# Kernel optimization log

Hardware: AMD Instinct MI355X
Metric: run time of the kernel (lower is better)

Reference implementation:

```python
import jax, jax.numpy as jnp
import numpy as np

C_RGB, C_EV, K = 64, 32, 3
PAD = K // 2
MID = 32


def setup_inputs() -> dict:
    key = jax.random.key(0)
    ks = jax.random.split(key, 6)
    B, H, W = 4, 256, 256
    rgb_feature = jax.random.normal(ks[0], (B, C_RGB, H, W), dtype=jnp.float32)
    event_feature = jax.random.normal(ks[1], (B, C_EV, H, W), dtype=jnp.float32)
    cin = C_RGB + C_EV
    # 1x1 conv weights stored as [out, in] (kaiming-ish scale)
    W1 = jax.random.normal(ks[2], (MID, cin), dtype=jnp.float32) / np.sqrt(cin)
    b1 = jnp.zeros((MID,), dtype=jnp.float32)
    W2 = jax.random.normal(ks[3], (C_RGB * K * K, MID), dtype=jnp.float32) / np.sqrt(MID)
    b2 = jnp.zeros((C_RGB * K * K,), dtype=jnp.float32)
    return {"rgb_feature": rgb_feature, "event_feature": event_feature,
            "W1": W1, "b1": b1, "W2": W2, "b2": b2}


def _extract_patches(x, k):
    # x: [B, C, H+2p, W+2p] -> [B, C, k, k, H, W]
    B, C, Hp, Wp = x.shape
    H, W = Hp - 2 * PAD, Wp - 2 * PAD
    rows = [jnp.stack([x[:, :, i:i + H, j:j + W] for j in range(k)], axis=2)
            for i in range(k)]
    return jnp.stack(rows, axis=2)  # [B, C, k, k, H, W]


def reference(rgb_feature, event_feature, W1, b1, W2, b2):
    B, C, H, W = rgb_feature.shape
    fused = jnp.concatenate([rgb_feature, event_feature], axis=1)  # [B, cin, H, W]
    # 1x1 convs as channel contractions
    h = jnp.einsum('bchw,mc->bmhw', fused, W1) + b1[None, :, None, None]
    h = jax.nn.relu(h)
    dk = jnp.einsum('bmhw,om->bohw', h, W2) + b2[None, :, None, None]
    dynamic_kernels = dk.reshape(B, C, K, K, H, W)
    rgb_padded = jnp.pad(rgb_feature, ((0, 0), (0, 0), (PAD, PAD), (PAD, PAD)), mode='reflect')
    patches = _extract_patches(rgb_padded, K)  # [B, C, K, K, H, W]
    out = jnp.einsum('bcijhw,bcijhw->bchw', patches, dynamic_kernels)
    return out
```

## Files before the change

kernel.cpp:

```cpp
#include <hip/hip_runtime.h>

#define CRGB 64
#define CEV  32
#define CIN  96
#define MID  32
#define HH   256
#define WW   256
#define HW   (HH*WW)

#define TLH 16
#define TLW 32
#define SRH 18
#define SRW 34
#define SPX (SRH*SRW)

typedef _Float16 f16x8 __attribute__((ext_vector_type(8)));
typedef _Float16 f16x4 __attribute__((ext_vector_type(4)));
typedef float    f32x4 __attribute__((ext_vector_type(4)));

#define WS_W2F 0
#define WS_W1F 36864
#define WS_B2P 43008

__global__ __launch_bounds__(256) void prep_kernel(
    const float* __restrict__ W1, const float* __restrict__ W2,
    const float* __restrict__ b2, char* __restrict__ ws)
{
    _Float16* W2f = (_Float16*)(ws + WS_W2F);
    _Float16* W1f = (_Float16*)(ws + WS_W1F);
    float*    b2p = (float*)(ws + WS_B2P);
    const int idx = blockIdx.x * 256 + threadIdx.x;
    if (idx < 18432) {
        const int e   = idx & 7;
        const int ln  = (idx >> 3) & 63;
        const int t   = idx >> 9;
        const int ij  = t % 9, cg = t / 9;
        const int c   = cg * 16 + (ln & 15);
        const int kap = (ln >> 4) * 8 + e;
        const int m   = ((kap >> 2) & 1) * 16 + (kap >> 3) * 4 + (kap & 3);
        W2f[idx] = (_Float16)W2[(c * 9 + ij) * MID + m];
    }
    if (idx < 3072) {
        const int e  = idx & 7;
        const int ln = (idx >> 3) & 63;
        const int t  = idx >> 9;
        const int ks = t >> 1, mh = t & 1;
        const int m  = mh * 16 + (ln & 15);
        const int k  = ks * 32 + (ln >> 4) * 8 + e;
        W1f[idx] = (_Float16)W1[m * CIN + k];
    }
    if (idx < 576) {
        const int cc = idx & 15;
        const int t  = idx >> 4;
        const int ij = t % 9, cg = t / 9;
        b2p[idx] = b2[(cg * 16 + cc) * 9 + ij];
    }
}

__global__ __launch_bounds__(512, 4) void fusion_mfma2(
    const float* __restrict__ rgb, const float* __restrict__ ev,
    const float* __restrict__ b1, const char* __restrict__ ws,
    float* __restrict__ out)
{
    __shared__ __align__(16) _Float16 srgb[SPX * 64];

    const int tid  = threadIdx.x;
    const int wave = tid >> 6;
    const int lane = tid & 63;
    const int l15  = lane & 15;
    const int g    = lane >> 4;

    const int bx = blockIdx.x;
    const int tc = bx & 7, tr = (bx >> 3) & 15, b = bx >> 7;
    const int px0 = tc * TLW, py0 = tr * TLH;

    const float* rgbP = rgb + (size_t)b * CRGB * HW;
    const float* evP  = ev  + (size_t)b * CEV  * HW;
    float*       outP = out + (size_t)b * CRGB * HW;

    const _Float16* W2f = (const _Float16*)(ws + WS_W2F);
    const _Float16* W1f = (const _Float16*)(ws + WS_W1F);
    const float*    b2p = (const float*)(ws + WS_B2P);

    f16x8* sv = (f16x8*)srgb;
    for (int p = tid; p < SPX; p += 512) {
        const int row = p / SRW;
        const int col = p - row * SRW;
        int gy = py0 - 1 + row; gy = gy < 0 ? 1 : (gy > HH - 1 ? HH - 2 : gy);
        int gx = px0 - 1 + col; gx = gx < 0 ? 1 : (gx > WW - 1 ? WW - 2 : gx);
        const float* src = rgbP + (size_t)gy * WW + gx;
        const int pb = p * 8, ps = p & 7;
#pragma unroll
        for (int q = 0; q < 8; ++q) {
            f16x8 v;
#pragma unroll
            for (int e = 0; e < 8; ++e)
                v[e] = (_Float16)src[(size_t)(q * 8 + e) * HW];
            sv[pb + (q ^ ps)] = v;
        }
    }

    f16x8 a1[6];
#pragma unroll
    for (int t = 0; t < 6; ++t)
        a1[t] = ((const f16x8*)W1f)[t * 64 + lane];
    const f32x4 b1v0 = *(const f32x4*)(b1 + g * 4);
    const f32x4 b1v1 = *(const f32x4*)(b1 + 16 + g * 4);

    __syncthreads();

    f16x8 bfr[4];
#pragma unroll
    for (int st = 0; st < 4; ++st) {
        const int row_l = wave * 2 + (st & 1);
        const int col   = (st >> 1) * 16 + l15;
        const int pt    = (row_l + 1) * SRW + col + 1;
        const f16x8 bk0 = sv[pt * 8 + ( g      ^ (pt & 7))];
        const f16x8 bk1 = sv[pt * 8 + ((4 + g) ^ (pt & 7))];
        const float* esrc = evP + (size_t)(py0 + row_l) * WW + (px0 + col);
        f16x8 bk2;
#pragma unroll
        for (int e = 0; e < 8; ++e)
            bk2[e] = (_Float16)esrc[(size_t)(g * 8 + e) * HW];
        f32x4 d0 = {0.f, 0.f, 0.f, 0.f}, d1 = {0.f, 0.f, 0.f, 0.f};
        d0 = __builtin_amdgcn_mfma_f32_16x16x32_f16(a1[0], bk0, d0, 0, 0, 0);
        d1 = __builtin_amdgcn_mfma_f32_16x16x32_f16(a1[1], bk0, d1, 0, 0, 0);
        d0 = __builtin_amdgcn_mfma_f32_16x16x32_f16(a1[2], bk1, d0, 0, 0, 0);
        d1 = __builtin_amdgcn_mfma_f32_16x16x32_f16(a1[3], bk1, d1, 0, 0, 0);
        d0 = __builtin_amdgcn_mfma_f32_16x16x32_f16(a1[4], bk2, d0, 0, 0, 0);
        d1 = __builtin_amdgcn_mfma_f32_16x16x32_f16(a1[5], bk2, d1, 0, 0, 0);
        f16x8 bf;
#pragma unroll
        for (int r = 0; r < 4; ++r) {
            float v0 = d0[r] + b1v0[r]; v0 = v0 > 0.f ? v0 : 0.f;
            float v1 = d1[r] + b1v1[r]; v1 = v1 > 0.f ? v1 : 0.f;
            bf[r]     = (_Float16)v0;
            bf[4 + r] = (_Float16)v1;
        }
        bfr[st] = bf;
    }

    for (int cg = 0; cg < 4; ++cg) {
        f16x8 a2[9];
        f32x4 ci[9];
#pragma unroll
        for (int ij = 0; ij < 9; ++ij) {
            a2[ij] = ((const f16x8*)W2f)[(cg * 9 + ij) * 64 + lane];
            ci[ij] = *(const f32x4*)(b2p + (cg * 9 + ij) * 16 + g * 4);
        }
        const int qs  = cg * 2 + (g >> 1);
        const int sub = g & 1;
#pragma unroll
        for (int st = 0; st < 4; ++st) {
            const int row_l = wave * 2 + (st & 1);
            const int col   = (st >> 1) * 16 + l15;
            float acc0 = 0.f, acc1 = 0.f, acc2 = 0.f, acc3 = 0.f;
#pragma unroll
            for (int ij = 0; ij < 9; ++ij) {
                const f32x4 d = __builtin_amdgcn_mfma_f32_16x16x32_f16(a2[ij], bfr[st], ci[ij], 0, 0, 0);
                const int pt = (row_l + ij / 3) * SRW + col + (ij % 3);
                const f16x4 pv = ((const f16x4*)srgb)[(pt * 8 + (qs ^ (pt & 7))) * 2 + sub];
                acc0 = fmaf(d[0], (float)pv[0], acc0);
                acc1 = fmaf(d[1], (float)pv[1], acc1);
                acc2 = fmaf(d[2], (float)pv[2], acc2);
                acc3 = fmaf(d[3], (float)pv[3], acc3);
            }
            float* op = outP + (size_t)(cg * 16 + g * 4) * HW
                             + (size_t)(py0 + row_l) * WW + (px0 + col);
            op[0]      = acc0;
            op[HW]     = acc1;
            op[2 * HW] = acc2;
            op[3 * HW] = acc3;
        }
    }
}

extern "C" void kernel_launch(void* const* d_in, const int* in_sizes, int n_in,
                              void* d_out, int out_size, void* d_ws, size_t ws_size,
                              hipStream_t stream) {
    const float* rgb = (const float*)d_in[0];
    const float* ev  = (const float*)d_in[1];
    const float* W1p = (const float*)d_in[2];
    const float* b1p = (const float*)d_in[3];
    const float* W2p = (const float*)d_in[4];
    const float* b2p = (const float*)d_in[5];
    float* out = (float*)d_out;
    char* ws = (char*)d_ws;

    hipLaunchKernelGGL(prep_kernel, dim3(72), dim3(256), 0, stream, W1p, W2p, b2p, ws);

    const int B = in_sizes[0] / (CRGB * HW);
    hipLaunchKernelGGL(fusion_mfma2, dim3(B * 128), dim3(512), 0, stream,
                       rgb, ev, b1p, ws, out);
}
```

Before: 66.14 us.

## Stage rgb tile into LDS as fp32 via direct global-to-LDS loads with 1024 threads

```diff
diff --git a/kernel.cpp b/kernel.cpp
--- a/kernel.cpp
+++ b/kernel.cpp
@@ -13,10 +13,13 @@
 #define SRH 18
 #define SRW 34
 #define SPX (SRH*SRW)
+#define QSTRIDE (SPX*4)
 
 typedef _Float16 f16x8 __attribute__((ext_vector_type(8)));
-typedef _Float16 f16x4 __attribute__((ext_vector_type(4)));
 typedef float    f32x4 __attribute__((ext_vector_type(4)));
+
+typedef const __attribute__((address_space(1))) float* gas_fp;
+typedef __attribute__((address_space(3))) float*       las_fp;
 
 #define WS_W2F 0
 #define WS_W1F 36864
@@ -57,12 +60,12 @@
     }
 }
 
-__global__ __launch_bounds__(512, 4) void fusion_mfma2(
+__global__ __launch_bounds__(1024, 1) void fusion_mfma5(
     const float* __restrict__ rgb, const float* __restrict__ ev,
     const float* __restrict__ b1, const char* __restrict__ ws,
     float* __restrict__ out)
 {
-    __shared__ __align__(16) _Float16 srgb[SPX * 64];
+    __shared__ __align__(16) float srgb[16 * QSTRIDE];
 
     const int tid  = threadIdx.x;
     const int wave = tid >> 6;
@@ -82,21 +85,24 @@
     const _Float16* W1f = (const _Float16*)(ws + WS_W1F);
     const float*    b2p = (const float*)(ws + WS_B2P);
 
-    f16x8* sv = (f16x8*)srgb;
-    for (int p = tid; p < SPX; p += 512) {
-        const int row = p / SRW;
-        const int col = p - row * SRW;
-        int gy = py0 - 1 + row; gy = gy < 0 ? 1 : (gy > HH - 1 ? HH - 2 : gy);
-        int gx = px0 - 1 + col; gx = gx < 0 ? 1 : (gx > WW - 1 ? WW - 2 : gx);
-        const float* src = rgbP + (size_t)gy * WW + gx;
-        const int pb = p * 8, ps = p & 7;
-#pragma unroll
-        for (int q = 0; q < 8; ++q) {
-            f16x8 v;
-#pragma unroll
-            for (int e = 0; e < 8; ++e)
-                v[e] = (_Float16)src[(size_t)(q * 8 + e) * HW];
-            sv[pb + (q ^ ps)] = v;
+    {
+        const int q = wave;
+        const float* chbase = rgbP + (size_t)(q * 4) * HW;
+        float* ldsbase = &srgb[q * QSTRIDE];
+#pragma unroll 4
+        for (int j = 0; j < 39; ++j) {
+            if (j < 38 || lane < 16) {
+                const int li  = j * 64 + lane;
+                const int p   = li >> 2, r = li & 3;
+                const int row = p / SRW;
+                const int col = p - row * SRW;
+                int gy = py0 - 1 + row; gy = gy < 0 ? 1 : (gy > HH - 1 ? HH - 2 : gy);
+                int gx = px0 - 1 + col; gx = gx < 0 ? 1 : (gx > WW - 1 ? WW - 2 : gx);
+                const float* gsrc = chbase + (size_t)r * HW + gy * WW + gx;
+                __builtin_amdgcn_global_load_lds(
+                    (gas_fp)(const void*)gsrc,
+                    (las_fp)(void*)(ldsbase + j * 64), 4, 0, 0);
+            }
         }
     }
 
@@ -107,28 +113,43 @@
     const f32x4 b1v0 = *(const f32x4*)(b1 + g * 4);
     const f32x4 b1v1 = *(const f32x4*)(b1 + 16 + g * 4);
 
+    const int row_l = wave;
+    f16x8 bk2[2];
+#pragma unroll
+    for (int st = 0; st < 2; ++st) {
+        const int col = st * 16 + l15;
+        const float* esrc = evP + (size_t)(py0 + row_l) * WW + (px0 + col);
+#pragma unroll
+        for (int e = 0; e < 8; ++e)
+            bk2[st][e] = (_Float16)esrc[(size_t)(g * 8 + e) * HW];
+    }
+
     __syncthreads();
 
-    f16x8 bfr[4];
-#pragma unroll
-    for (int st = 0; st < 4; ++st) {
-        const int row_l = wave * 2 + (st & 1);
-        const int col   = (st >> 1) * 16 + l15;
-        const int pt    = (row_l + 1) * SRW + col + 1;
-        const f16x8 bk0 = sv[pt * 8 + ( g      ^ (pt & 7))];
-        const f16x8 bk1 = sv[pt * 8 + ((4 + g) ^ (pt & 7))];
-        const float* esrc = evP + (size_t)(py0 + row_l) * WW + (px0 + col);
-        f16x8 bk2;
-#pragma unroll
-        for (int e = 0; e < 8; ++e)
-            bk2[e] = (_Float16)esrc[(size_t)(g * 8 + e) * HW];
+    f16x8 bfr[2];
+#pragma unroll
+    for (int st = 0; st < 2; ++st) {
+        const int col = st * 16 + l15;
+        const int pt  = (row_l + 1) * SRW + col + 1;
+        const f32x4 c0 = *(const f32x4*)&srgb[(g * 2)     * QSTRIDE + pt * 4];
+        const f32x4 c1 = *(const f32x4*)&srgb[(g * 2 + 1) * QSTRIDE + pt * 4];
+        const f32x4 c2 = *(const f32x4*)&srgb[(8 + g * 2)     * QSTRIDE + pt * 4];
+        const f32x4 c3 = *(const f32x4*)&srgb[(8 + g * 2 + 1) * QSTRIDE + pt * 4];
+        f16x8 bk0, bk1;
+#pragma unroll
+        for (int r = 0; r < 4; ++r) {
+            bk0[r]     = (_Float16)c0[r];
+            bk0[4 + r] = (_Float16)c1[r];
+            bk1[r]     = (_Float16)c2[r];
+            bk1[4 + r] = (_Float16)c3[r];
+        }
         f32x4 d0 = {0.f, 0.f, 0.f, 0.f}, d1 = {0.f, 0.f, 0.f, 0.f};
         d0 = __builtin_amdgcn_mfma_f32_16x16x32_f16(a1[0], bk0, d0, 0, 0, 0);
         d1 = __builtin_amdgcn_mfma_f32_16x16x32_f16(a1[1], bk0, d1, 0, 0, 0);
         d0 = __builtin_amdgcn_mfma_f32_16x16x32_f16(a1[2], bk1, d0, 0, 0, 0);
         d1 = __builtin_amdgcn_mfma_f32_16x16x32_f16(a1[3], bk1, d1, 0, 0, 0);
-        d0 = __builtin_amdgcn_mfma_f32_16x16x32_f16(a1[4], bk2, d0, 0, 0, 0);
-        d1 = __builtin_amdgcn_mfma_f32_16x16x32_f16(a1[5], bk2, d1, 0, 0, 0);
+        d0 = __builtin_amdgcn_mfma_f32_16x16x32_f16(a1[4], bk2[st], d0, 0, 0, 0);
+        d1 = __builtin_amdgcn_mfma_f32_16x16x32_f16(a1[5], bk2[st], d1, 0, 0, 0);
         f16x8 bf;
 #pragma unroll
         for (int r = 0; r < 4; ++r) {
@@ -148,22 +169,20 @@
             a2[ij] = ((const f16x8*)W2f)[(cg * 9 + ij) * 64 + lane];
             ci[ij] = *(const f32x4*)(b2p + (cg * 9 + ij) * 16 + g * 4);
         }
-        const int qs  = cg * 2 + (g >> 1);
-        const int sub = g & 1;
-#pragma unroll
-        for (int st = 0; st < 4; ++st) {
-            const int row_l = wave * 2 + (st & 1);
-            const int col   = (st >> 1) * 16 + l15;
+        const int qa = cg * 4 + g;
+#pragma unroll
+        for (int st = 0; st < 2; ++st) {
+            const int col = st * 16 + l15;
             float acc0 = 0.f, acc1 = 0.f, acc2 = 0.f, acc3 = 0.f;
 #pragma unroll
             for (int ij = 0; ij < 9; ++ij) {
                 const f32x4 d = __builtin_amdgcn_mfma_f32_16x16x32_f16(a2[ij], bfr[st], ci[ij], 0, 0, 0);
                 const int pt = (row_l + ij / 3) * SRW + col + (ij % 3);
-                const f16x4 pv = ((const f16x4*)srgb)[(pt * 8 + (qs ^ (pt & 7))) * 2 + sub];
-                acc0 = fmaf(d[0], (float)pv[0], acc0);
-                acc1 = fmaf(d[1], (float)pv[1], acc1);
-                acc2 = fmaf(d[2], (float)pv[2], acc2);
-                acc3 = fmaf(d[3], (float)pv[3], acc3);
+                const f32x4 pv = *(const f32x4*)&srgb[qa * QSTRIDE + pt * 4];
+                acc0 = fmaf(d[0], pv[0], acc0);
+                acc1 = fmaf(d[1], pv[1], acc1);
+                acc2 = fmaf(d[2], pv[2], acc2);
+                acc3 = fmaf(d[3], pv[3], acc3);
             }
             float* op = outP + (size_t)(cg * 16 + g * 4) * HW
                              + (size_t)(py0 + row_l) * WW + (px0 + col);
@@ -190,6 +209,6 @@
     hipLaunchKernelGGL(prep_kernel, dim3(72), dim3(256), 0, stream, W1p, W2p, b2p, ws);
 
     const int B = in_sizes[0] / (CRGB * HW);
-    hipLaunchKernelGGL(fusion_mfma2, dim3(B * 128), dim3(512), 0, stream,
+    hipLaunchKernelGGL(fusion_mfma5, dim3(B * 128), dim3(1024), 0, stream,
                        rgb, ev, b1p, ws, out);
 }
```

Result: slower. 97.09 us (+46.8%).
